# Performance work log

Hardware: AMD Instinct MI355X
Metric: run time of the kernel (lower is better)

## Reference

```python
import jax, jax.numpy as jnp
import numpy as np

B, S = 256, 512
NQ = 1000           # n_skills
MEM, DK, DV, FC = 20, 50, 200, 50  # memory_size, key dim, value dim, final fc dim


def _kaiming(key, shape, fan_in):
    return jax.random.normal(key, shape) * np.float32(np.sqrt(2.0 / fan_in))


def setup_inputs() -> dict:
    key = jax.random.key(0)
    ks = jax.random.split(key, 12)
    q_data = jax.random.randint(ks[0], (B, S), 0, NQ + 1)
    qa_data = jax.random.randint(ks[1], (B, S), 0, 2 * NQ + 1)
    u = jax.random.uniform(ks[2], (B * S,))
    # target: -1 = masked/padding, else binary label (matches target.ge(0) masking)
    target = jnp.where(u < 0.1, -1.0, (u > 0.55).astype(jnp.float32))
    q_embed_w = _kaiming(ks[3], (NQ + 1, DK), DK)
    qa_embed_w = _kaiming(ks[4], (2 * NQ + 1, DV), DV)
    memory_key = _kaiming(ks[5], (MEM, DK), DK)
    init_memory_value = _kaiming(ks[6], (MEM, DV), DV)
    erase_w = _kaiming(ks[7], (DV, DV), DV)
    erase_b = jnp.zeros((DV,), jnp.float32)
    add_w = _kaiming(ks[8], (DV, DV), DV)
    add_b = jnp.zeros((DV,), jnp.float32)
    read_w = _kaiming(ks[9], (DV + FC, FC), DV + FC)
    read_b = jnp.zeros((FC,), jnp.float32)
    pred_w = _kaiming(ks[10], (FC, 1), FC)
    pred_b = jnp.zeros((1,), jnp.float32)
    return dict(q_data=q_data, qa_data=qa_data, target=target,
                q_embed_w=q_embed_w, qa_embed_w=qa_embed_w,
                memory_key=memory_key, init_memory_value=init_memory_value,
                erase_w=erase_w, erase_b=erase_b, add_w=add_w, add_b=add_b,
                read_w=read_w, read_b=read_b, pred_w=pred_w, pred_b=pred_b)


def reference(q_data, qa_data, target, q_embed_w, qa_embed_w, memory_key,
              init_memory_value, erase_w, erase_b, add_w, add_b,
              read_w, read_b, pred_w, pred_b):
    b = q_data.shape[0]
    q_e = q_embed_w[q_data]     # [B,S,DK]
    qa_e = qa_embed_w[qa_data]  # [B,S,DV]
    Mv0 = jnp.broadcast_to(init_memory_value, (b, MEM, DV))

    def step(Mv, xs):
        q_t, qa_t = xs                                        # [B,DK], [B,DV]
        corr = jax.nn.softmax(q_t @ memory_key.T, axis=1)     # [B,MEM] addressing
        read = jnp.einsum('bm,bmd->bd', corr, Mv)             # weighted read
        erase = jax.nn.sigmoid(qa_t @ erase_w + erase_b)      # [B,DV]
        add = jnp.tanh(qa_t @ add_w + add_b)                  # [B,DV]
        w = corr[:, :, None]                                  # [B,MEM,1]
        Mv = Mv * (1.0 - w * erase[:, None, :]) + w * add[:, None, :]
        return Mv, read

    _, reads = jax.lax.scan(step, Mv0, (q_e.transpose(1, 0, 2), qa_e.transpose(1, 0, 2)))
    reads = reads.transpose(1, 0, 2)                          # [B,S,DV]
    x = jnp.concatenate([reads, q_e], axis=-1)                # [B,S,DV+FC]
    h = jnp.tanh(x @ read_w + read_b)                         # [B,S,FC]
    logits = (h @ pred_w + pred_b).reshape(-1)                # [B*S]
    mask = target >= 0.0
    t = jnp.where(mask, target, 0.0)
    # numerically-stable BCE-with-logits, masked mean
    bce = jnp.maximum(logits, 0.0) - logits * t + jnp.log1p(jnp.exp(-jnp.abs(logits)))
    loss = jnp.sum(jnp.where(mask, bce, 0.0)) / jnp.maximum(mask.sum(), 1)
    return loss, jax.nn.sigmoid(logits)
```

## Files before the change

kernel.cpp:

```cpp
#include <hip/hip_runtime.h>
#include <math.h>

#define B_   256
#define S_   512
#define NQ_  1000
#define MEM_ 20
#define DK_  50
#define DV_  200
#define FC_  50
#define RPB  4
#define CHK  16
#define CLEN (S_/CHK)
#define NKS  7
#define XS_STRIDE 232
#define CORRF_STRIDE 24
#define NB_EA    ((2*NQ_+1+RPB-1)/RPB)
#define NB_CORR  4
#define NB_WPACK 7
#define NB_HQ    251
#define PREP_BLOCKS (NB_EA+NB_CORR+NB_WPACK+NB_HQ)

typedef __attribute__((ext_vector_type(8))) short bf16x8_t;
typedef __attribute__((ext_vector_type(4))) float f32x4_t;
typedef __attribute__((ext_vector_type(2))) float f32x2_t;

static __device__ __forceinline__ f32x2_t pkfma32(f32x2_t a, f32x2_t b, f32x2_t c){
  return __builtin_elementwise_fma(a, b, c);
}
static __device__ __forceinline__ unsigned short f2bf(float f){
  unsigned u = __float_as_uint(f);
  unsigned r = u + 0x7fffu + ((u >> 16) & 1u);
  return (unsigned short)(r >> 16);
}
static __device__ __forceinline__ float ftanh(float x){
  float e = __expf(2.f*x);
  return 1.f - 2.f*__builtin_amdgcn_rcpf(e+1.f);
}
static __device__ __forceinline__ float fsigm(float x){
  return __builtin_amdgcn_rcpf(1.f+__expf(-x));
}

#define RFL(x) __builtin_amdgcn_readfirstlane(x)

struct corr20 { float4 v0, v1, v2, v3, v4; };

__global__ __launch_bounds__(256) void k_prep1(
    const float* __restrict__ qaw,
    const float* __restrict__ ew, const float* __restrict__ eb,
    const float* __restrict__ aw, const float* __restrict__ ab,
    float2* __restrict__ eaTabF,
    const float* __restrict__ qw, const float* __restrict__ mk,
    float* __restrict__ corrF,
    const float* __restrict__ rw, const float* __restrict__ rb,
    const float* __restrict__ pw,
    unsigned short* __restrict__ WpFrag, float* __restrict__ pwPad,
    float* __restrict__ hq){
  __shared__ float qa[RPB*DV_];
  int blk = blockIdx.x;
  if(blk < NB_EA){
    int row0 = blk*RPB;
    for(int i=threadIdx.x; i<RPB*DV_; i+=256){
      int r = i/DV_, cc = i - r*DV_;
      int row = row0 + r;
      qa[i] = (row <= 2*NQ_) ? qaw[row*DV_+cc] : 0.f;
    }
    __syncthreads();
    int d = threadIdx.x;
    if(d >= DV_) return;
    float accE[RPB], accA[RPB];
    #pragma unroll
    for(int r=0;r<RPB;++r){ accE[r] = eb[d]; accA[r] = ab[d]; }
    float we0 = ew[d], wa0 = aw[d];
    for(int j=0;j<DV_;++j){
      int jn = (j+1 < DV_) ? j+1 : j;
      float we1 = ew[jn*DV_+d];
      float wa1 = aw[jn*DV_+d];
      #pragma unroll
      for(int r=0;r<RPB;++r){
        float x = qa[r*DV_+j];
        accE[r] = fmaf(x, we0, accE[r]);
        accA[r] = fmaf(x, wa0, accA[r]);
      }
      we0 = we1; wa0 = wa1;
    }
    #pragma unroll
    for(int r=0;r<RPB;++r){
      int row = row0 + r;
      if(row <= 2*NQ_)
        eaTabF[(size_t)row*DV_+d] = make_float2(fsigm(accE[r]), ftanh(accA[r]));
    }
  } else if(blk < NB_EA+NB_CORR){
    int q = (blk-NB_EA)*256 + threadIdx.x;
    if(q > NQ_) return;
    float qv[DK_];
    #pragma unroll
    for(int j=0;j<DK_;++j) qv[j] = qw[q*DK_+j];
    float s[MEM_]; float mx = -1e30f;
    #pragma unroll
    for(int m=0;m<MEM_;++m){
      float acc = 0.f;
      #pragma unroll
      for(int j=0;j<DK_;++j) acc = fmaf(qv[j], mk[m*DK_+j], acc);
      s[m] = acc; mx = fmaxf(mx, acc);
    }
    float sum = 0.f;
    #pragma unroll
    for(int m=0;m<MEM_;++m){ s[m] = __expf(s[m]-mx); sum += s[m]; }
    float inv = __builtin_amdgcn_rcpf(sum);
    #pragma unroll
    for(int m=0;m<MEM_;++m) corrF[q*CORRF_STRIDE+m] = s[m]*inv;
  } else if(blk < NB_EA+NB_CORR+NB_WPACK){
    int ks = blk - (NB_EA+NB_CORR);
    int nt = threadIdx.x >> 6;
    int lane = threadIdx.x & 63;
    int quad = lane >> 4, col = lane & 15;
    int n = nt*16 + col;
    unsigned short tmp[8];
    #pragma unroll
    for(int j=0;j<8;++j){
      int k = ks*32 + quad*8 + j;
      tmp[j] = (k < DV_ && n < FC_) ? f2bf(rw[k*FC_+n]) : (unsigned short)0;
    }
    uint4* dst = reinterpret_cast<uint4*>(WpFrag + ((size_t)(ks*4+nt)*64 + lane)*8);
    *dst = *reinterpret_cast<const uint4*>(tmp);
    if(ks == 0 && threadIdx.x < 64)
      pwPad[threadIdx.x] = (threadIdx.x < FC_) ? pw[threadIdx.x] : 0.f;
  } else {
    int idx = (blk-(NB_EA+NB_CORR+NB_WPACK))*256 + threadIdx.x;
    int q = idx >> 6, n = idx & 63;
    if(q > NQ_) return;
    float v = 0.f;
    if(n < FC_){
      float acc = rb[n];
      #pragma unroll
      for(int j=0;j<DK_;++j)
        acc = fmaf(qw[q*DK_+j], rw[(DV_+j)*FC_+n], acc);
      v = acc;
    }
    hq[q*64+n] = v;
  }
}

__global__ __launch_bounds__(256,1) void k_seq(const int* __restrict__ qd,
    const int* __restrict__ qad,
    const float* __restrict__ corrF,
    const float2* __restrict__ eaTabF,
    const float* __restrict__ mv0,
    const unsigned short* __restrict__ WpFrag,
    const float* __restrict__ hq,
    const float* __restrict__ pwPad, const float* __restrict__ pb,
    const float* __restrict__ target,
    float* __restrict__ out, float2* __restrict__ partials){
  __shared__ unsigned short Xs[CLEN*XS_STRIDE];
  __shared__ float sred[2][2][16];
  __shared__ float sbce[4];

  const int b = blockIdx.x;
  const int d = threadIdx.x;
  const int dc = (d < DV_) ? d : DV_-1;
  const bool act = (d < DV_);
  const bool padw = (d < 224);
  const int* __restrict__ qp  = qd  + b*S_;
  const int* __restrict__ qap = qad + b*S_;

  const int wave = threadIdx.x >> 6;
  const int lane = threadIdx.x & 63;
  const int col  = lane & 15, quad = lane >> 4;
  const int rt   = wave & 1;
  const int nh   = wave >> 1;
  const int mbase = rt*16;

  f32x2_t Mv[MEM_/2];
  #pragma unroll
  for(int i=0;i<MEM_/2;++i)
    Mv[i] = (f32x2_t){ mv0[(2*i)*DV_+dc], mv0[(2*i+1)*DV_+dc] };

  #define LD_EAF(DST, ROW) { int _r = RFL(ROW); DST = eaTabF[(size_t)_r*DV_ + dc]; }
  #define LD_CORRF(CS, QV) { const float4* _p = (const float4*)(corrF + (size_t)(QV)*CORRF_STRIDE); \
    CS.v0=_p[0]; CS.v1=_p[1]; CS.v2=_p[2]; CS.v3=_p[3]; CS.v4=_p[4]; }

  float2 ea0, ea1, ea2, ea3;
  LD_EAF(ea0, qap[0])  LD_EAF(ea1, qap[1])  LD_EAF(ea2, qap[2])  LD_EAF(ea3, qap[3])
  corr20 cs0, cs1, cs2, cs3;
  { int t0=qp[0], t1=qp[1], t2=qp[2], t3=qp[3];
    LD_CORRF(cs0, t0) LD_CORRF(cs1, t1) LD_CORRF(cs2, t2) LD_CORRF(cs3, t3) }
  int qa_i0=qap[4], qa_i1=qap[5], qa_i2=qap[6], qa_i3=qap[7];
  int qv_i0=qp[4],  qv_i1=qp[5],  qv_i2=qp[6],  qv_i3=qp[7];

  int qpreC[4];
  #pragma unroll
  for(int reg=0;reg<4;++reg) qpreC[reg] = qp[mbase + quad*4 + reg];
  float pwv[2];
  #pragma unroll
  for(int j=0;j<2;++j) pwv[j] = pwPad[(nh*2+j)*16 + col];
  const float pbv = pb[0];

  float bceAcc = 0.f, cntAcc = 0.f;

  #define PAIR(CPX, CPY, i) { \
    f32x2_t cp = {CPX, CPY}; \
    racc = pkfma32(cp, Mv[i], racc); \
    f32x2_t tt_ = pkfma32(-Mv[i], ee, aa); \
    Mv[i] = pkfma32(cp, tt_, Mv[i]); }
  #define STEP(TT_, EA, CS) { \
    f32x2_t ee = {EA.x, EA.x}, aa = {EA.y, EA.y}; \
    f32x2_t racc = {0.f, 0.f}; \
    PAIR(CS.v0.x, CS.v0.y, 0) PAIR(CS.v0.z, CS.v0.w, 1) \
    PAIR(CS.v1.x, CS.v1.y, 2) PAIR(CS.v1.z, CS.v1.w, 3) \
    PAIR(CS.v2.x, CS.v2.y, 4) PAIR(CS.v2.z, CS.v2.w, 5) \
    PAIR(CS.v3.x, CS.v3.y, 6) PAIR(CS.v3.z, CS.v3.w, 7) \
    PAIR(CS.v4.x, CS.v4.y, 8) PAIR(CS.v4.z, CS.v4.w, 9) \
    float rd = racc[0] + racc[1]; \
    if(padw) Xs[(TT_)*XS_STRIDE + d] = act ? f2bf(rd) : (unsigned short)0; }
  #define SLOT(K, EAr, CSr, QAr, QVr) { \
    STEP(tt+(K), EAr, CSr) \
    LD_EAF(EAr, QAr) \
    LD_CORRF(CSr, QVr) \
    { int g8 = c*CLEN + tt + (K) + 8; int ix = (g8 < S_) ? g8 : S_-1; \
      QAr = qap[ix]; QVr = qp[ix]; } }

  #pragma unroll 1
  for(int c=0;c<CHK;++c){
    int qpreN[4];
    { int cn = (c+1 < CHK) ? c+1 : c;
      #pragma unroll
      for(int reg=0;reg<4;++reg) qpreN[reg] = qp[cn*CLEN + mbase + quad*4 + reg]; }

    #pragma unroll 1
    for(int tt=0; tt<CLEN; tt+=4){
      SLOT(0, ea0, cs0, qa_i0, qv_i0)
      SLOT(1, ea1, cs1, qa_i1, qv_i1)
      SLOT(2, ea2, cs2, qa_i2, qv_i2)
      SLOT(3, ea3, cs3, qa_i3, qv_i3)
    }

    float hqv[4][2];
    #pragma unroll
    for(int reg=0;reg<4;++reg)
      #pragma unroll
      for(int j=0;j<2;++j)
        hqv[reg][j] = hq[qpreC[reg]*64 + (nh*2+j)*16 + col];

    __syncthreads();

    f32x4_t acc[2];
    acc[0] = (f32x4_t){0.f,0.f,0.f,0.f};
    acc[1] = (f32x4_t){0.f,0.f,0.f,0.f};
    #pragma unroll
    for(int ks=0;ks<NKS;++ks){
      bf16x8_t a = *reinterpret_cast<const bf16x8_t*>(Xs + (mbase+col)*XS_STRIDE + quad*8 + ks*32);
      #pragma unroll
      for(int j=0;j<2;++j){
        int nt = nh*2 + j;
        bf16x8_t bfr = *reinterpret_cast<const bf16x8_t*>(WpFrag + ((size_t)(ks*4+nt)*64 + lane)*8);
        acc[j] = __builtin_amdgcn_mfma_f32_16x16x32_bf16(a, bfr, acc[j], 0, 0, 0);
      }
    }

    float part[4];
    #pragma unroll
    for(int reg=0;reg<4;++reg){
      float s = 0.f;
      #pragma unroll
      for(int j=0;j<2;++j){
        float h = acc[j][reg] + hqv[reg][j];
        s = fmaf(pwv[j], ftanh(h), s);
      }
      part[reg] = s;
    }
    #pragma unroll
    for(int off=1; off<16; off<<=1){
      #pragma unroll
      for(int reg=0;reg<4;++reg) part[reg] += __shfl_xor(part[reg], off, 64);
    }
    if(col == 0){
      #pragma unroll
      for(int reg=0;reg<4;++reg) sred[rt][nh][quad*4+reg] = part[reg];
    }
    __syncthreads();

    if(nh == 0 && col == 0){
      #pragma unroll
      for(int reg=0;reg<4;++reg){
        int idx = quad*4 + reg;
        int mloc = mbase + idx;
        int row = b*S_ + c*CLEN + mloc;
        float logit = sred[rt][0][idx] + sred[rt][1][idx] + pbv;
        out[1+row] = fsigm(logit);
        float t = target[row];
        if(t >= 0.f){
          cntAcc += 1.f;
          bceAcc += fmaxf(logit,0.f) - logit*t + log1pf(__expf(-fabsf(logit)));
        }
      }
    }
    #pragma unroll
    for(int reg=0;reg<4;++reg) qpreC[reg] = qpreN[reg];
  }
  #undef SLOT
  #undef STEP
  #undef PAIR
  #undef LD_CORRF
  #undef LD_EAF

  bceAcc += __shfl_xor(bceAcc, 16, 64); cntAcc += __shfl_xor(cntAcc, 16, 64);
  bceAcc += __shfl_xor(bceAcc, 32, 64); cntAcc += __shfl_xor(cntAcc, 32, 64);
  if(lane == 0 && nh == 0){ sbce[wave] = bceAcc; sbce[2+wave] = cntAcc; }
  __syncthreads();
  if(threadIdx.x == 0)
    partials[b] = make_float2(sbce[0]+sbce[1], sbce[2]+sbce[3]);
}

__global__ __launch_bounds__(256) void k_fin(const float2* __restrict__ partials,
                                             float* __restrict__ out){
  float2 p = partials[threadIdx.x];
  float bce = p.x, cnt = p.y;
  #pragma unroll
  for(int off=32; off>0; off>>=1){
    bce += __shfl_down(bce, off, 64);
    cnt += __shfl_down(cnt, off, 64);
  }
  __shared__ float sb[4], sc[4];
  int w = threadIdx.x >> 6;
  if((threadIdx.x & 63) == 0){ sb[w] = bce; sc[w] = cnt; }
  __syncthreads();
  if(threadIdx.x == 0){
    float Bt = sb[0]+sb[1]+sb[2]+sb[3];
    float Ct = sc[0]+sc[1]+sc[2]+sc[3];
    out[0] = Bt / fmaxf(Ct, 1.f);
  }
}

extern "C" void kernel_launch(void* const* d_in, const int* in_sizes, int n_in,
                              void* d_out, int out_size, void* d_ws, size_t ws_size,
                              hipStream_t stream){
  const int*   qd     = (const int*)d_in[0];
  const int*   qad    = (const int*)d_in[1];
  const float* target = (const float*)d_in[2];
  const float* qw     = (const float*)d_in[3];
  const float* qaw    = (const float*)d_in[4];
  const float* mk     = (const float*)d_in[5];
  const float* mv0    = (const float*)d_in[6];
  const float* ew     = (const float*)d_in[7];
  const float* eb     = (const float*)d_in[8];
  const float* aw     = (const float*)d_in[9];
  const float* ab     = (const float*)d_in[10];
  const float* rw     = (const float*)d_in[11];
  const float* rb     = (const float*)d_in[12];
  const float* pw     = (const float*)d_in[13];
  const float* pb     = (const float*)d_in[14];
  float* out = (float*)d_out;

  char* ws = (char*)d_ws;
  size_t off = 0;
  float2* partials = (float2*)(ws + off);            off += (((size_t)B_*8 + 255)/256)*256;
  float* corrF    = (float*)(ws + off);              off += (((size_t)(NQ_+1)*CORRF_STRIDE*4 + 255)/256)*256;
  float2* eaTabF  = (float2*)(ws + off);             off += (((size_t)(2*NQ_+1)*DV_*8 + 255)/256)*256;
  unsigned short* WpFrag = (unsigned short*)(ws + off); off += ((size_t)NKS*4*64*8*2 + 255)/256*256;
  float* pwPad    = (float*)(ws + off);              off += 256;
  float* hq       = (float*)(ws + off);              off += (size_t)(NQ_+1)*64*4;

  k_prep1<<<dim3(PREP_BLOCKS), dim3(256), 0, stream>>>(qaw, ew, eb, aw, ab, eaTabF,
                                                       qw, mk, corrF,
                                                       rw, rb, pw, WpFrag, pwPad, hq);
  k_seq<<<dim3(B_), dim3(256), 0, stream>>>(qd, qad, corrF, eaTabF, mv0,
                                            WpFrag, hq, pwPad, pb, target, out, partials);
  k_fin<<<dim3(1), dim3(256), 0, stream>>>(partials, out);
}
```

Before: 243.8 us.

## Stage per-chunk erase/add and addressing rows into double-buffered LDS, pack erase/add as fp16

The sequential scan kernel now copies the whole question index arrays into shared memory. For each chunk it cooperatively gathers that chunk's erase/add rows and softmax addressing rows from global memory into a double-buffered LDS area while the previous chunk computes. The inner recurrence then reads from LDS instead of issuing dependent global loads each step. The erase/add table is packed as two fp16 values per 32-bit word, which halves its footprint and bandwidth but lowers precision. The addressing table stride is tightened to 20, and the read accumulation is split into two chains to shorten dependency latency.

```diff
diff --git a/kernel.cpp b/kernel.cpp
--- a/kernel.cpp
+++ b/kernel.cpp
@@ -13,7 +13,7 @@
 #define CLEN (S_/CHK)
 #define NKS  7
 #define XS_STRIDE 232
-#define CORRF_STRIDE 24
+#define CRS  20
 #define NB_EA    ((2*NQ_+1+RPB-1)/RPB)
 #define NB_CORR  4
 #define NB_WPACK 7
@@ -23,7 +23,9 @@
 typedef __attribute__((ext_vector_type(8))) short bf16x8_t;
 typedef __attribute__((ext_vector_type(4))) float f32x4_t;
 typedef __attribute__((ext_vector_type(2))) float f32x2_t;
-
+typedef __attribute__((ext_vector_type(2))) _Float16 f16x2_t;
+
+static __device__ __forceinline__ f16x2_t h2(unsigned u){ return __builtin_bit_cast(f16x2_t, u); }
 static __device__ __forceinline__ f32x2_t pkfma32(f32x2_t a, f32x2_t b, f32x2_t c){
   return __builtin_elementwise_fma(a, b, c);
 }
@@ -40,15 +42,11 @@
   return __builtin_amdgcn_rcpf(1.f+__expf(-x));
 }
 
-#define RFL(x) __builtin_amdgcn_readfirstlane(x)
-
-struct corr20 { float4 v0, v1, v2, v3, v4; };
-
 __global__ __launch_bounds__(256) void k_prep1(
     const float* __restrict__ qaw,
     const float* __restrict__ ew, const float* __restrict__ eb,
     const float* __restrict__ aw, const float* __restrict__ ab,
-    float2* __restrict__ eaTabF,
+    unsigned* __restrict__ eaTab,
     const float* __restrict__ qw, const float* __restrict__ mk,
     float* __restrict__ corrF,
     const float* __restrict__ rw, const float* __restrict__ rb,
@@ -86,8 +84,11 @@
     #pragma unroll
     for(int r=0;r<RPB;++r){
       int row = row0 + r;
-      if(row <= 2*NQ_)
-        eaTabF[(size_t)row*DV_+d] = make_float2(fsigm(accE[r]), ftanh(accA[r]));
+      if(row <= 2*NQ_){
+        unsigned he = (unsigned)__builtin_bit_cast(unsigned short, (_Float16)fsigm(accE[r]));
+        unsigned ha = (unsigned)__builtin_bit_cast(unsigned short, (_Float16)ftanh(accA[r]));
+        eaTab[(size_t)row*DV_+d] = he | (ha << 16);
+      }
     }
   } else if(blk < NB_EA+NB_CORR){
     int q = (blk-NB_EA)*256 + threadIdx.x;
@@ -108,7 +109,7 @@
     for(int m=0;m<MEM_;++m){ s[m] = __expf(s[m]-mx); sum += s[m]; }
     float inv = __builtin_amdgcn_rcpf(sum);
     #pragma unroll
-    for(int m=0;m<MEM_;++m) corrF[q*CORRF_STRIDE+m] = s[m]*inv;
+    for(int m=0;m<MEM_;++m) corrF[(size_t)q*CRS+m] = s[m]*inv;
   } else if(blk < NB_EA+NB_CORR+NB_WPACK){
     int ks = blk - (NB_EA+NB_CORR);
     int nt = threadIdx.x >> 6;
@@ -144,14 +145,17 @@
 __global__ __launch_bounds__(256,1) void k_seq(const int* __restrict__ qd,
     const int* __restrict__ qad,
     const float* __restrict__ corrF,
-    const float2* __restrict__ eaTabF,
+    const unsigned* __restrict__ eaTab,
     const float* __restrict__ mv0,
     const unsigned short* __restrict__ WpFrag,
     const float* __restrict__ hq,
     const float* __restrict__ pwPad, const float* __restrict__ pb,
     const float* __restrict__ target,
     float* __restrict__ out, float2* __restrict__ partials){
+  __shared__ __align__(16) unsigned eaL[2][CLEN*DV_];
+  __shared__ __align__(16) float    crL[2][CLEN*CRS];
   __shared__ unsigned short Xs[CLEN*XS_STRIDE];
+  __shared__ int qpL[S_], qapL[S_];
   __shared__ float sred[2][2][16];
   __shared__ float sbce[4];
 
@@ -160,8 +164,6 @@
   const int dc = (d < DV_) ? d : DV_-1;
   const bool act = (d < DV_);
   const bool padw = (d < 224);
-  const int* __restrict__ qp  = qd  + b*S_;
-  const int* __restrict__ qap = qad + b*S_;
 
   const int wave = threadIdx.x >> 6;
   const int lane = threadIdx.x & 63;
@@ -170,77 +172,117 @@
   const int nh   = wave >> 1;
   const int mbase = rt*16;
 
+  {
+    const int* qp_g  = qd  + b*S_;
+    const int* qap_g = qad + b*S_;
+    #pragma unroll
+    for(int i=0;i<S_/256;++i){
+      qpL[d + 256*i]  = qp_g[d + 256*i];
+      qapL[d + 256*i] = qap_g[d + 256*i];
+    }
+  }
+  __syncthreads();
+
   f32x2_t Mv[MEM_/2];
   #pragma unroll
   for(int i=0;i<MEM_/2;++i)
     Mv[i] = (f32x2_t){ mv0[(2*i)*DV_+dc], mv0[(2*i+1)*DV_+dc] };
 
-  #define LD_EAF(DST, ROW) { int _r = RFL(ROW); DST = eaTabF[(size_t)_r*DV_ + dc]; }
-  #define LD_CORRF(CS, QV) { const float4* _p = (const float4*)(corrF + (size_t)(QV)*CORRF_STRIDE); \
-    CS.v0=_p[0]; CS.v1=_p[1]; CS.v2=_p[2]; CS.v3=_p[3]; CS.v4=_p[4]; }
-
-  float2 ea0, ea1, ea2, ea3;
-  LD_EAF(ea0, qap[0])  LD_EAF(ea1, qap[1])  LD_EAF(ea2, qap[2])  LD_EAF(ea3, qap[3])
-  corr20 cs0, cs1, cs2, cs3;
-  { int t0=qp[0], t1=qp[1], t2=qp[2], t3=qp[3];
-    LD_CORRF(cs0, t0) LD_CORRF(cs1, t1) LD_CORRF(cs2, t2) LD_CORRF(cs3, t3) }
-  int qa_i0=qap[4], qa_i1=qap[5], qa_i2=qap[6], qa_i3=qap[7];
-  int qv_i0=qp[4],  qv_i1=qp[5],  qv_i2=qp[6],  qv_i3=qp[7];
-
-  int qpreC[4];
-  #pragma unroll
-  for(int reg=0;reg<4;++reg) qpreC[reg] = qp[mbase + quad*4 + reg];
+  unsigned eaStg[25]; float crStg[3];
+  #define STAGE_ISSUE(CI) { \
+    _Pragma("unroll") \
+    for(int j=0;j<25;++j){ \
+      int k = d + 256*j; \
+      int t = (int)(((unsigned)k*41944u)>>23); \
+      int dd = k - t*200; \
+      int row = qapL[(CI)*CLEN + t]; \
+      eaStg[j] = eaTab[(size_t)row*DV_ + dd]; \
+    } \
+    _Pragma("unroll") \
+    for(int j=0;j<3;++j){ \
+      int k = d + 256*j; \
+      if(k < CLEN*CRS){ \
+        int t = (int)(((unsigned)k*3277u)>>16); \
+        int dd = k - t*CRS; \
+        int row = qpL[(CI)*CLEN + t]; \
+        crStg[j] = corrF[(size_t)row*CRS + dd]; \
+      } \
+    } }
+  #define STAGE_WRITE(BUF) { \
+    _Pragma("unroll") \
+    for(int j=0;j<25;++j) eaL[BUF][d + 256*j] = eaStg[j]; \
+    _Pragma("unroll") \
+    for(int j=0;j<3;++j){ int k = d + 256*j; if(k < CLEN*CRS) crL[BUF][k] = crStg[j]; } }
+
+  STAGE_ISSUE(0)
+  STAGE_WRITE(0)
+
   float pwv[2];
   #pragma unroll
   for(int j=0;j<2;++j) pwv[j] = pwPad[(nh*2+j)*16 + col];
   const float pbv = pb[0];
-
   float bceAcc = 0.f, cntAcc = 0.f;
-
-  #define PAIR(CPX, CPY, i) { \
-    f32x2_t cp = {CPX, CPY}; \
-    racc = pkfma32(cp, Mv[i], racc); \
+  __syncthreads();
+
+  #define LDC(SET, T_) { const float4* p_ = (const float4*)&crC[(T_)*CRS]; \
+    SET##0 = p_[0]; SET##1 = p_[1]; SET##2 = p_[2]; SET##3 = p_[3]; SET##4 = p_[4]; }
+  #define LDEA(R, T_) { R = eaC[(T_)*DV_ + dc]; }
+  #define PAIR(CPV, i, RA) { \
+    f32x2_t cp = CPV; \
+    RA = pkfma32(cp, Mv[i], RA); \
     f32x2_t tt_ = pkfma32(-Mv[i], ee, aa); \
     Mv[i] = pkfma32(cp, tt_, Mv[i]); }
-  #define STEP(TT_, EA, CS) { \
-    f32x2_t ee = {EA.x, EA.x}, aa = {EA.y, EA.y}; \
-    f32x2_t racc = {0.f, 0.f}; \
-    PAIR(CS.v0.x, CS.v0.y, 0) PAIR(CS.v0.z, CS.v0.w, 1) \
-    PAIR(CS.v1.x, CS.v1.y, 2) PAIR(CS.v1.z, CS.v1.w, 3) \
-    PAIR(CS.v2.x, CS.v2.y, 4) PAIR(CS.v2.z, CS.v2.w, 5) \
-    PAIR(CS.v3.x, CS.v3.y, 6) PAIR(CS.v3.z, CS.v3.w, 7) \
-    PAIR(CS.v4.x, CS.v4.y, 8) PAIR(CS.v4.z, CS.v4.w, 9) \
-    float rd = racc[0] + racc[1]; \
-    if(padw) Xs[(TT_)*XS_STRIDE + d] = act ? f2bf(rd) : (unsigned short)0; }
-  #define SLOT(K, EAr, CSr, QAr, QVr) { \
-    STEP(tt+(K), EAr, CSr) \
-    LD_EAF(EAr, QAr) \
-    LD_CORRF(CSr, QVr) \
-    { int g8 = c*CLEN + tt + (K) + 8; int ix = (g8 < S_) ? g8 : S_-1; \
-      QAr = qap[ix]; QVr = qp[ix]; } }
+  #define STEP(T_, EAU, S0,S1,S2,S3,S4) { \
+    f16x2_t pe = h2(EAU); \
+    float e32 = (float)pe[0], a32 = (float)pe[1]; \
+    f32x2_t ee = {e32,e32}, aa = {a32,a32}; \
+    f32x2_t r0 = {0.f,0.f}, r1 = {0.f,0.f}; \
+    PAIR(((f32x2_t){S0.x,S0.y}), 0, r0) PAIR(((f32x2_t){S0.z,S0.w}), 1, r1) \
+    PAIR(((f32x2_t){S1.x,S1.y}), 2, r0) PAIR(((f32x2_t){S1.z,S1.w}), 3, r1) \
+    PAIR(((f32x2_t){S2.x,S2.y}), 4, r0) PAIR(((f32x2_t){S2.z,S2.w}), 5, r1) \
+    PAIR(((f32x2_t){S3.x,S3.y}), 6, r0) PAIR(((f32x2_t){S3.z,S3.w}), 7, r1) \
+    PAIR(((f32x2_t){S4.x,S4.y}), 8, r0) PAIR(((f32x2_t){S4.z,S4.w}), 9, r1) \
+    float rd = (r0[0]+r0[1]) + (r1[0]+r1[1]); \
+    if(padw) Xs[(T_)*XS_STRIDE + d] = act ? f2bf(rd) : (unsigned short)0; }
 
   #pragma unroll 1
   for(int c=0;c<CHK;++c){
-    int qpreN[4];
-    { int cn = (c+1 < CHK) ? c+1 : c;
-      #pragma unroll
-      for(int reg=0;reg<4;++reg) qpreN[reg] = qp[cn*CLEN + mbase + quad*4 + reg]; }
+    const unsigned* eaC = eaL[c&1];
+    const float*    crC = crL[c&1];
+
+    int qpre[4]; float hqv[4][2];
+    #pragma unroll
+    for(int reg=0;reg<4;++reg) qpre[reg] = qpL[c*CLEN + mbase + quad*4 + reg];
+    #pragma unroll
+    for(int reg=0;reg<4;++reg)
+      #pragma unroll
+      for(int j=0;j<2;++j)
+        hqv[reg][j] = hq[qpre[reg]*64 + (nh*2+j)*16 + col];
+
+    if(c+1 < CHK) STAGE_ISSUE(c+1)
+
+    unsigned ea0, ea1, ea2, ea3;
+    LDEA(ea0, 0) LDEA(ea1, 1) LDEA(ea2, 2) LDEA(ea3, 3)
+    float4 crA0,crA1,crA2,crA3,crA4, crB0,crB1,crB2,crB3,crB4;
+    LDC(crA, 0) LDC(crB, 1)
 
     #pragma unroll 1
     for(int tt=0; tt<CLEN; tt+=4){
-      SLOT(0, ea0, cs0, qa_i0, qv_i0)
-      SLOT(1, ea1, cs1, qa_i1, qv_i1)
-      SLOT(2, ea2, cs2, qa_i2, qv_i2)
-      SLOT(3, ea3, cs3, qa_i3, qv_i3)
-    }
-
-    float hqv[4][2];
-    #pragma unroll
-    for(int reg=0;reg<4;++reg)
-      #pragma unroll
-      for(int j=0;j<2;++j)
-        hqv[reg][j] = hq[qpreC[reg]*64 + (nh*2+j)*16 + col];
-
+      STEP(tt+0, ea0, crA0,crA1,crA2,crA3,crA4)
+      LDC(crA, tt+2)
+      { int nx = tt+4; nx = (nx<CLEN)?nx:CLEN-1; LDEA(ea0, nx) }
+      STEP(tt+1, ea1, crB0,crB1,crB2,crB3,crB4)
+      LDC(crB, tt+3)
+      { int nx = tt+5; nx = (nx<CLEN)?nx:CLEN-1; LDEA(ea1, nx) }
+      STEP(tt+2, ea2, crA0,crA1,crA2,crA3,crA4)
+      { int nx = tt+4; nx = (nx<CLEN)?nx:CLEN-1; LDC(crA, nx) }
+      { int nx = tt+6; nx = (nx<CLEN)?nx:CLEN-1; LDEA(ea2, nx) }
+      STEP(tt+3, ea3, crB0,crB1,crB2,crB3,crB4)
+      { int nx = tt+5; nx = (nx<CLEN)?nx:CLEN-1; LDC(crB, nx) }
+      { int nx = tt+7; nx = (nx<CLEN)?nx:CLEN-1; LDEA(ea3, nx) }
+    }
+
+    if(c+1 < CHK) STAGE_WRITE((c+1)&1)
     __syncthreads();
 
     f32x4_t acc[2];
@@ -294,14 +336,13 @@
         }
       }
     }
-    #pragma unroll
-    for(int reg=0;reg<4;++reg) qpreC[reg] = qpreN[reg];
   }
-  #undef SLOT
   #undef STEP
   #undef PAIR
-  #undef LD_CORRF
-  #undef LD_EAF
+  #undef LDEA
+  #undef LDC
+  #undef STAGE_WRITE
+  #undef STAGE_ISSUE
 
   bceAcc += __shfl_xor(bceAcc, 16, 64); cntAcc += __shfl_xor(cntAcc, 16, 64);
   bceAcc += __shfl_xor(bceAcc, 32, 64); cntAcc += __shfl_xor(cntAcc, 32, 64);
@@ -354,16 +395,16 @@
   char* ws = (char*)d_ws;
   size_t off = 0;
   float2* partials = (float2*)(ws + off);            off += (((size_t)B_*8 + 255)/256)*256;
-  float* corrF    = (float*)(ws + off);              off += (((size_t)(NQ_+1)*CORRF_STRIDE*4 + 255)/256)*256;
-  float2* eaTabF  = (float2*)(ws + off);             off += (((size_t)(2*NQ_+1)*DV_*8 + 255)/256)*256;
+  float* corrF    = (float*)(ws + off);              off += (((size_t)(NQ_+1)*CRS*4 + 255)/256)*256;
+  unsigned* eaTab = (unsigned*)(ws + off);           off += (((size_t)(2*NQ_+1)*DV_*4 + 255)/256)*256;
   unsigned short* WpFrag = (unsigned short*)(ws + off); off += ((size_t)NKS*4*64*8*2 + 255)/256*256;
   float* pwPad    = (float*)(ws + off);              off += 256;
   float* hq       = (float*)(ws + off);              off += (size_t)(NQ_+1)*64*4;
 
-  k_prep1<<<dim3(PREP_BLOCKS), dim3(256), 0, stream>>>(qaw, ew, eb, aw, ab, eaTabF,
+  k_prep1<<<dim3(PREP_BLOCKS), dim3(256), 0, stream>>>(qaw, ew, eb, aw, ab, eaTab,
                                                        qw, mk, corrF,
                                                        rw, rb, pw, WpFrag, pwPad, hq);
-  k_seq<<<dim3(B_), dim3(256), 0, stream>>>(qd, qad, corrF, eaTabF, mv0,
+  k_seq<<<dim3(B_), dim3(256), 0, stream>>>(qd, qad, corrF, eaTab, mv0,
                                             WpFrag, hq, pwPad, pb, target, out, partials);
   k_fin<<<dim3(1), dim3(256), 0, stream>>>(partials, out);
 }
```

After: 254.0 us. 1.04x slower.
